# Kernel tuning notes

Measured on AMD Instinct MI355X. Metric: run time of the kernel, lower is better.

The kernel has to match this reference:

```python
import jax, jax.numpy as jnp
import numpy as np

N = 200000   # num_nodes
D = 64       # embedding_dims
B = 4096     # batch of target nodes (batched per-edge processing)
K = 128      # padded in-neighbor count per target
W = 20       # window_size (history deque length)
H = 128      # hidden_size


def setup_inputs() -> dict:
    key = jax.random.key(0)
    ks = jax.random.split(key, 14)
    return {
        "adj_time": jax.random.uniform(ks[0], (N,), jnp.float32),          # last-seen times in [0,1)
        "gc": jax.random.uniform(ks[1], (N,), jnp.float32),                 # per-node centrality scalar (dict_gc)
        "cur_time": jnp.ones((1,), jnp.float32),                            # current event time (>= all stored times)
        "neigh_mask": jnp.ones((B, K), jnp.float32),                        # 1 = valid neighbor slot
        "hist_feat": jax.random.normal(ks[2], (B, W, 2 * D), jnp.float32),  # feature_dict[...]['feature'] deque
        "hist_time": jax.random.uniform(ks[3], (B, W), jnp.float32),        # feature_dict[...]['time'] deque
        "t2v_w": jax.random.normal(ks[4], (D,), jnp.float32),               # Time2Vec('cos') weights
        "t2v_b": jax.random.normal(ks[5], (D,), jnp.float32),
        "node_w": jax.random.normal(ks[6], (D,), jnp.float32),              # linear_node: Linear(1, D)
        "node_b": jax.random.normal(ks[7], (D,), jnp.float32),
        "att_w": jax.random.normal(ks[8], (2 * D,), jnp.float32),           # Attention: score = cat(a,b) @ w + b
        "att_b": jax.random.normal(ks[9], (1,), jnp.float32),
        "weight": jax.random.normal(ks[10], (H, 4 * D), jnp.float32) * 0.05,
        "targets": jax.random.randint(ks[11], (B,), 0, N),
        "neigh_idx": jax.random.randint(ks[12], (B, K), 0, N),
    }


def reference(adj_time, gc, cur_time, neigh_mask, hist_feat, hist_time,
              t2v_w, t2v_b, node_w, node_b, att_w, att_b, weight,
              targets, neigh_idx):
    t = cur_time[0]

    def node_encoding(idx):
        # Time2Vec('cos'): first channel linear, rest cos(w*dt+b)
        dt = jnp.abs(t - adj_time[idx])[..., None]            # [..., 1]
        phase = t2v_w * dt + t2v_b                            # [..., D]
        tv = jnp.concatenate([phase[..., :1], jnp.cos(phase[..., 1:])], axis=-1)
        feat = jax.nn.relu(tv + gc[idx][..., None] * node_w + node_b)
        # F.normalize (L2 over feature dim)
        return feat / jnp.maximum(jnp.linalg.norm(feat, axis=-1, keepdims=True), 1e-12)

    tgt_feat = node_encoding(targets)       # [B, D]
    ngh_feat = node_encoding(neigh_idx)     # [B, K, D]

    # Decayer(2, 'log'): time_score = 1 / (2 * log(e + dt))
    time_score = 1.0 / (2.0 * jnp.log(jnp.e + (t - adj_time[neigh_idx])))   # [B, K]
    # Attention score between target and each neighbor encoding
    att = (tgt_feat @ att_w[:D])[:, None] \
        + jnp.einsum("bkd,d->bk", ngh_feat, att_w[D:]) + att_b[0]           # [B, K]
    score = jax.nn.leaky_relu(time_score + att, 0.01) * neigh_mask          # [B, K]
    neigh_agg = jnp.einsum("bk,bkd->bd", score, ngh_feat)                   # [B, D]

    combined = jnp.concatenate([tgt_feat, neigh_agg], axis=-1)              # [B, 2D]

    # History aggregation with Decayer(2, 'rev'): w = 1 / (2 * (1 + dt))
    hist_w = 1.0 / (2.0 * (1.0 + (t - hist_time)))                          # [B, W]
    hist_agg = jnp.einsum("bw,bwd->bd", hist_w, hist_feat)                  # [B, 2D]

    feat4 = jnp.concatenate([hist_agg, combined], axis=-1)                  # [B, 4D]
    return jax.nn.relu(feat4 @ weight.T)                                    # [B, H]
```

## Files before the change

### kernel.cpp

```cpp
#include <hip/hip_runtime.h>
#include <math.h>

#define NN 200000
#define DD 64
#define BB 4096
#define KK 128
#define WW 20
#define HH 128
#define TPB 512
#define RPB 4

#define INV2PI 0.15915494309189535f

__device__ __forceinline__ float fast_rcp(float x) { return __builtin_amdgcn_rcpf(x); }
__device__ __forceinline__ float fast_rsq(float x) { return __builtin_amdgcn_rsqf(x); }

__global__ __launch_bounds__(512, 8) void fused(
    const float* __restrict__ adj_time, const float* __restrict__ gc,
    const float* __restrict__ cur_time, const float* __restrict__ neigh_mask,
    const float* __restrict__ hist_feat, const float* __restrict__ hist_time,
    const float* __restrict__ t2v_w, const float* __restrict__ t2v_b,
    const float* __restrict__ node_w, const float* __restrict__ node_b,
    const float* __restrict__ att_w, const float* __restrict__ att_b,
    const float* __restrict__ weight,
    const int* __restrict__ targets, const int* __restrict__ neigh_idx,
    float* __restrict__ out)
{
    const int b0   = blockIdx.x * RPB;
    const int tid  = threadIdx.x;
    const int lane = tid & 63;
    const int wv   = tid >> 6;

    __shared__ float4 dtg[RPB * KK];
    __shared__ float  stL[RPB];
    __shared__ float  p3p[RPB][DD];
    __shared__ float  tile[RPB * 256];

    const float t = cur_time[0];

    const int   slot = tid;
    const int   idx  = neigh_idx[b0 * KK + slot];
    const float m    = neigh_mask[b0 * KK + slot];
    const float at   = adj_time[idx];
    const float g    = gc[idx];
    const float dt   = fabsf(t - at);
    const float ts   = fast_rcp(2.0f * __logf(2.71828182845904523536f + (t - at)));
    dtg[slot] = make_float4(dt, g, 0.f, 0.f);

    if (tid >= 384) {
        const int r  = (tid >> 5) & 3;
        const int c4 = tid & 31;
        const float*  ht = hist_time + (size_t)(b0 + r) * WW;
        const float4* hf = (const float4*)(hist_feat + (size_t)(b0 + r) * WW * 128) + c4;
        float4 s4 = make_float4(0.f, 0.f, 0.f, 0.f);
#pragma unroll 4
        for (int w = 0; w < WW; ++w) {
            float  hw = fast_rcp(2.0f * (1.0f + (t - ht[w])));
            float4 v  = hf[w * 32];
            s4.x = fmaf(hw, v.x, s4.x);
            s4.y = fmaf(hw, v.y, s4.y);
            s4.z = fmaf(hw, v.z, s4.z);
            s4.w = fmaf(hw, v.w, s4.w);
        }
        *(float4*)(tile + r * 256 + c4 * 4) = s4;
    }

    if (wv < RPB) {
        int   tg  = targets[b0 + wv];
        float dtT = fabsf(t - adj_time[tg]);
        float gT  = gc[tg];
        float ph  = fmaf(t2v_w[lane], dtT, t2v_b[lane]);
        float tv_ = (lane == 0) ? ph : __cosf(ph);
        float f   = fmaxf(tv_ + fmaf(gT, node_w[lane], node_b[lane]), 0.f);
        float ss  = f * f;
#pragma unroll
        for (int off = 32; off; off >>= 1) ss += __shfl_xor(ss, off, 64);
        float invn = fast_rsq(fmaxf(ss, 1e-24f));
        float tfn  = f * invn;
        float sdt  = tfn * att_w[lane];
#pragma unroll
        for (int off = 32; off; off >>= 1) sdt += __shfl_xor(sdt, off, 64);
        if (lane == 0) stL[wv] = sdt;
        tile[wv * 256 + 128 + lane] = tfn;
    }

    float s2, sd;
    {
        {
            float ph = fmaf(t2v_w[0], dt, t2v_b[0]);
            float f  = fmaxf(ph + fmaf(g, node_w[0], node_b[0]), 0.f);
            s2 = f * f;
            sd = f * att_w[64];
        }
#pragma unroll 4
        for (int d = 1; d < 64; ++d) {
            float ph = fmaf(t2v_w[d], dt, t2v_b[d]);
            float f  = fmaxf(__cosf(ph) + fmaf(g, node_w[d], node_b[d]), 0.f);
            s2 = fmaf(f, f, s2);
            sd = fmaf(f, att_w[64 + d], sd);
        }
    }
    __syncthreads();

    {
        float invn = fast_rsq(fmaxf(s2, 1e-24f));
        float sc   = ts + stL[slot >> 7] + sd * invn + att_b[0];
        sc = (sc > 0.f) ? sc : 0.01f * sc;
        dtg[slot].z = sc * m * invn;
    }
    __syncthreads();

    const int r3   = wv >> 1;
    const int half = wv & 1;
    float acc3 = 0.f;
    {
        float scn = (lane == 0) ? 1.f : INV2PI;
        float pw  = t2v_w[lane] * scn;
        float pb  = t2v_b[lane] * scn;
        float nw  = node_w[lane];
        float nb2 = node_b[lane];
        const int base = r3 * KK + half * 64;
#pragma unroll 4
        for (int k = 0; k < 64; ++k) {
            float4 dgw = dtg[base + k];
            float  ph  = fmaf(pw, dgw.x, pb);
            float  cv  = __builtin_amdgcn_cosf(ph);
            float  tv_ = lane ? cv : ph;
            float  f   = fmaxf(tv_ + fmaf(dgw.y, nw, nb2), 0.f);
            acc3 = fmaf(dgw.z, f, acc3);
        }
    }
    if (half) p3p[r3][lane] = acc3;
    __syncthreads();
    if (!half) tile[r3 * 256 + 192 + lane] = acc3 + p3p[r3][lane];
    __syncthreads();

    const int h  = tid & 127;
    const int sq = tid >> 7;
    const float4* w4 = (const float4*)weight + h * 64 + sq * 16;
    const int jb = sq * 64;
    float a0 = 0.f, a1 = 0.f, a2 = 0.f, a3 = 0.f;
#pragma unroll 4
    for (int j4 = 0; j4 < 16; ++j4) {
        float4 w  = w4[j4];
        const int jo = jb + j4 * 4;
        float4 f0 = *(const float4*)(tile + 0 * 256 + jo);
        float4 f1 = *(const float4*)(tile + 1 * 256 + jo);
        float4 f2 = *(const float4*)(tile + 2 * 256 + jo);
        float4 f3 = *(const float4*)(tile + 3 * 256 + jo);
        a0 += w.x * f0.x + w.y * f0.y + w.z * f0.z + w.w * f0.w;
        a1 += w.x * f1.x + w.y * f1.y + w.z * f1.z + w.w * f1.w;
        a2 += w.x * f2.x + w.y * f2.y + w.z * f2.z + w.w * f2.w;
        a3 += w.x * f3.x + w.y * f3.y + w.z * f3.z + w.w * f3.w;
    }

    float* prow = (float*)dtg;
    prow[(0 * 4 + sq) * 128 + h] = a0;
    prow[(1 * 4 + sq) * 128 + h] = a1;
    prow[(2 * 4 + sq) * 128 + h] = a2;
    prow[(3 * 4 + sq) * 128 + h] = a3;
    __syncthreads();
    {
        const int r2 = tid >> 7;
        float s = prow[(r2 * 4 + 0) * 128 + h] + prow[(r2 * 4 + 1) * 128 + h]
                + prow[(r2 * 4 + 2) * 128 + h] + prow[(r2 * 4 + 3) * 128 + h];
        out[(size_t)(b0 + r2) * 128 + h] = fmaxf(s, 0.f);
    }
}

extern "C" void kernel_launch(void* const* d_in, const int* in_sizes, int n_in,
                              void* d_out, int out_size, void* d_ws, size_t ws_size,
                              hipStream_t stream) {
    const float* adj_time  = (const float*)d_in[0];
    const float* gc        = (const float*)d_in[1];
    const float* cur_time  = (const float*)d_in[2];
    const float* neigh_mask= (const float*)d_in[3];
    const float* hist_feat = (const float*)d_in[4];
    const float* hist_time = (const float*)d_in[5];
    const float* t2v_w     = (const float*)d_in[6];
    const float* t2v_b     = (const float*)d_in[7];
    const float* node_w    = (const float*)d_in[8];
    const float* node_b    = (const float*)d_in[9];
    const float* att_w     = (const float*)d_in[10];
    const float* att_b     = (const float*)d_in[11];
    const float* weight    = (const float*)d_in[12];
    const int*   targets   = (const int*)d_in[13];
    const int*   neigh_idx = (const int*)d_in[14];

    float* out = (float*)d_out;

    fused<<<BB / RPB, TPB, 0, stream>>>(adj_time, gc, cur_time, neigh_mask,
                                        hist_feat, hist_time, t2v_w, t2v_b,
                                        node_w, node_b, att_w, att_b, weight,
                                        targets, neigh_idx, out);
}
```

Measured before the change: 133.9 us.

## Split history reduction across more threads, use raw cos, and retile final GEMV

The history aggregation now uses 256 threads, each summing half of the window, with the partial sums combined through shared memory after a sync. This shortens the serial per-thread load chain. Cosine evaluations switch to the hardware sin/cos instruction with pre-scaled phase, and the per-neighbor 63-step loop is fully unrolled. The output projection is retiled so each thread computes 2 rows by 2 hidden units, which changes the weight/tile reuse pattern. The trade-off is an extra shared buffer and combine step, and possibly more register pressure from full unrolling.

Result: slower. 164.9 us (+23.1%).

```diff
diff --git a/kernel.cpp b/kernel.cpp
--- a/kernel.cpp
+++ b/kernel.cpp
@@ -35,6 +35,7 @@
     __shared__ float  stL[RPB];
     __shared__ float  p3p[RPB][DD];
     __shared__ float  tile[RPB * 256];
+    __shared__ float4 hp[128];
 
     const float t = cur_time[0];
 
@@ -47,14 +48,18 @@
     const float ts   = fast_rcp(2.0f * __logf(2.71828182845904523536f + (t - at)));
     dtg[slot] = make_float4(dt, g, 0.f, 0.f);
 
-    if (tid >= 384) {
-        const int r  = (tid >> 5) & 3;
-        const int c4 = tid & 31;
-        const float*  ht = hist_time + (size_t)(b0 + r) * WW;
-        const float4* hf = (const float4*)(hist_feat + (size_t)(b0 + r) * WW * 128) + c4;
+    if (tid >= 256) {
+        const int i   = tid - 256;
+        const int col = i >> 1;
+        const int th  = i & 1;
+        const int r   = col >> 5;
+        const int c4  = col & 31;
+        const float*  ht = hist_time + (size_t)(b0 + r) * WW + th * 10;
+        const float4* hf = (const float4*)(hist_feat + (size_t)(b0 + r) * WW * 128)
+                         + c4 + th * 10 * 32;
         float4 s4 = make_float4(0.f, 0.f, 0.f, 0.f);
-#pragma unroll 4
-        for (int w = 0; w < WW; ++w) {
+#pragma unroll
+        for (int w = 0; w < 10; ++w) {
             float  hw = fast_rcp(2.0f * (1.0f + (t - ht[w])));
             float4 v  = hf[w * 32];
             s4.x = fmaf(hw, v.x, s4.x);
@@ -62,7 +67,8 @@
             s4.z = fmaf(hw, v.z, s4.z);
             s4.w = fmaf(hw, v.w, s4.w);
         }
-        *(float4*)(tile + r * 256 + c4 * 4) = s4;
+        if (th == 0) *(float4*)(tile + r * 256 + c4 * 4) = s4;
+        else         hp[col] = s4;
     }
 
     if (wv < RPB) {
@@ -70,7 +76,8 @@
         float dtT = fabsf(t - adj_time[tg]);
         float gT  = gc[tg];
         float ph  = fmaf(t2v_w[lane], dtT, t2v_b[lane]);
-        float tv_ = (lane == 0) ? ph : __cosf(ph);
+        float cv  = __builtin_amdgcn_cosf(ph * INV2PI);
+        float tv_ = (lane == 0) ? ph : cv;
         float f   = fmaxf(tv_ + fmaf(gT, node_w[lane], node_b[lane]), 0.f);
         float ss  = f * f;
 #pragma unroll
@@ -92,10 +99,11 @@
             s2 = f * f;
             sd = f * att_w[64];
         }
-#pragma unroll 4
+#pragma unroll
         for (int d = 1; d < 64; ++d) {
             float ph = fmaf(t2v_w[d], dt, t2v_b[d]);
-            float f  = fmaxf(__cosf(ph) + fmaf(g, node_w[d], node_b[d]), 0.f);
+            float cv = __builtin_amdgcn_cosf(ph * INV2PI);
+            float f  = fmaxf(cv + fmaf(g, node_w[d], node_b[d]), 0.f);
             s2 = fmaf(f, f, s2);
             sd = fmaf(f, att_w[64 + d], sd);
         }
@@ -109,6 +117,13 @@
         dtg[slot].z = sc * m * invn;
     }
     __syncthreads();
+
+    if (tid < 128) {
+        int r = tid >> 5, c4 = tid & 31;
+        float4* tp = (float4*)(tile + r * 256 + c4 * 4);
+        float4 a = *tp, b = hp[tid];
+        *tp = make_float4(a.x + b.x, a.y + b.y, a.z + b.z, a.w + b.w);
+    }
 
     const int r3   = wv >> 1;
     const int half = wv & 1;
@@ -135,33 +150,35 @@
     if (!half) tile[r3 * 256 + 192 + lane] = acc3 + p3p[r3][lane];
     __syncthreads();
 
-    const int h  = tid & 127;
-    const int sq = tid >> 7;
-    const float4* w4 = (const float4*)weight + h * 64 + sq * 16;
-    const int jb = sq * 64;
-    float a0 = 0.f, a1 = 0.f, a2 = 0.f, a3 = 0.f;
+    const int h2 = tid & 63;
+    const int sq = (tid >> 6) & 3;
+    const int rh = tid >> 8;
+    const float4* wA = (const float4*)weight + (h2     ) * 64 + sq * 16;
+    const float4* wB = (const float4*)weight + (h2 + 64) * 64 + sq * 16;
+    const float*  t0 = tile + (2 * rh    ) * 256 + sq * 64;
+    const float*  t1 = tile + (2 * rh + 1) * 256 + sq * 64;
+    float a00 = 0.f, a01 = 0.f, a10 = 0.f, a11 = 0.f;
 #pragma unroll 4
-    for (int j4 = 0; j4 < 16; ++j4) {
-        float4 w  = w4[j4];
-        const int jo = jb + j4 * 4;
-        float4 f0 = *(const float4*)(tile + 0 * 256 + jo);
-        float4 f1 = *(const float4*)(tile + 1 * 256 + jo);
-        float4 f2 = *(const float4*)(tile + 2 * 256 + jo);
-        float4 f3 = *(const float4*)(tile + 3 * 256 + jo);
-        a0 += w.x * f0.x + w.y * f0.y + w.z * f0.z + w.w * f0.w;
-        a1 += w.x * f1.x + w.y * f1.y + w.z * f1.z + w.w * f1.w;
-        a2 += w.x * f2.x + w.y * f2.y + w.z * f2.z + w.w * f2.w;
-        a3 += w.x * f3.x + w.y * f3.y + w.z * f3.z + w.w * f3.w;
+    for (int i = 0; i < 16; ++i) {
+        float4 wa = wA[i];
+        float4 wb = wB[i];
+        float4 f0 = *(const float4*)(t0 + i * 4);
+        float4 f1 = *(const float4*)(t1 + i * 4);
+        a00 += wa.x * f0.x + wa.y * f0.y + wa.z * f0.z + wa.w * f0.w;
+        a01 += wb.x * f0.x + wb.y * f0.y + wb.z * f0.z + wb.w * f0.w;
+        a10 += wa.x * f1.x + wa.y * f1.y + wa.z * f1.z + wa.w * f1.w;
+        a11 += wb.x * f1.x + wb.y * f1.y + wb.z * f1.z + wb.w * f1.w;
     }
 
     float* prow = (float*)dtg;
-    prow[(0 * 4 + sq) * 128 + h] = a0;
-    prow[(1 * 4 + sq) * 128 + h] = a1;
-    prow[(2 * 4 + sq) * 128 + h] = a2;
-    prow[(3 * 4 + sq) * 128 + h] = a3;
+    prow[((2 * rh    ) * 4 + sq) * 128 + h2     ] = a00;
+    prow[((2 * rh    ) * 4 + sq) * 128 + h2 + 64] = a01;
+    prow[((2 * rh + 1) * 4 + sq) * 128 + h2     ] = a10;
+    prow[((2 * rh + 1) * 4 + sq) * 128 + h2 + 64] = a11;
     __syncthreads();
     {
         const int r2 = tid >> 7;
+        const int h  = tid & 127;
         float s = prow[(r2 * 4 + 0) * 128 + h] + prow[(r2 * 4 + 1) * 128 + h]
                 + prow[(r2 * 4 + 2) * 128 + h] + prow[(r2 * 4 + 3) * 128 + h];
         out[(size_t)(b0 + r2) * 128 + h] = fmaxf(s, 0.f);
```
